# Kernel optimization log

Hardware: AMD Instinct MI355X
Metric: run time of the kernel (lower is better)

Reference implementation:

```python
import jax, jax.numpy as jnp
import numpy as np

BN_EPS = 1e-3


def _knn_group(p1, p2, k):
    # p1, p2: [B, N, 3]. For each point in p1, find k nearest in p2.
    d2 = (jnp.sum(p1 * p1, -1)[:, :, None]
          + jnp.sum(p2 * p2, -1)[:, None, :]
          - 2.0 * jnp.einsum('bnd,bmd->bnm', p1, p2))  # [B,N,N]
    _, idx = jax.lax.top_k(-d2, k)                      # [B,N,k]
    nn = jax.vmap(lambda pts, ind: pts[ind])(p2, idx)   # [B,N,k,3]
    resi = nn - p1[:, :, None, :]                       # [B,N,k,3]
    ss = jnp.sum(resi * resi, -1, keepdims=True)
    dist = jnp.sqrt(jnp.maximum(ss, 1e-12))             # safe norm
    feat = jnp.concatenate([resi, dist], -1)            # [B,N,k,4]
    return feat.transpose(0, 3, 1, 2), nn.transpose(0, 3, 1, 2)  # [B,4,N,k],[B,3,N,k]


def _conv_bn_relu(x, W, b, g, be, m, v):
    # 1x1 conv over channel dim: x [B,C,N,K], W [O,C]
    x = jnp.einsum('bcnk,oc->bonk', x, W) + b[None, :, None, None]
    x = (x - m[None, :, None, None]) * (g / jnp.sqrt(v + BN_EPS))[None, :, None, None] + be[None, :, None, None]
    return jax.nn.relu(x)


def setup_inputs() -> dict:
    key = jax.random.key(0)
    ks = jax.random.split(key, 20)
    B, N = 8, 2048
    chans = [4, 64, 64, 128]
    inp = {
        'points1': jax.random.normal(ks[0], (B, 3, N), jnp.float32),
        'points2': jax.random.normal(ks[1], (B, 3, N), jnp.float32),
    }
    for i in range(3):
        ci, co = chans[i], chans[i + 1]
        base = 2 + i * 6
        scale = 1.0 / np.sqrt(ci)
        inp[f'W{i+1}'] = jax.random.uniform(ks[base], (co, ci), jnp.float32, -scale, scale)
        inp[f'b{i+1}'] = jax.random.uniform(ks[base + 1], (co,), jnp.float32, -scale, scale)
        inp[f'g{i+1}'] = 1.0 + 0.1 * jax.random.normal(ks[base + 2], (co,), jnp.float32)
        inp[f'be{i+1}'] = 0.1 * jax.random.normal(ks[base + 3], (co,), jnp.float32)
        inp[f'm{i+1}'] = 0.05 * jax.random.normal(ks[base + 4], (co,), jnp.float32)
        inp[f'v{i+1}'] = jax.random.uniform(ks[base + 5], (co,), jnp.float32, 0.5, 1.5)
    inp['k'] = 32
    inp['t'] = 1
    return inp


def reference(points1, points2, W1, b1, g1, be1, m1, v1, W2, b2, g2, be2, m2, v2,
              W3, b3, g3, be3, m3, v3, k, t):
    p1 = points1.transpose(0, 2, 1)  # [B,N,3]
    p2 = points2.transpose(0, 2, 1)
    f1, nn1 = _knn_group(p1, p1, k)
    f2, nn2 = _knn_group(p1, p2, k)
    feats = jnp.concatenate([f1, f2], -1)          # [B,4,N,2k]
    grouped = jnp.concatenate([nn1, nn2], -1)      # [B,3,N,2k]
    x = _conv_bn_relu(feats, W1, b1, g1, be1, m1, v1)
    x = _conv_bn_relu(x, W2, b2, g2, be2, m2, v2)
    x = _conv_bn_relu(x, W3, b3, g3, be3, m3, v3)
    x = jnp.max(x, axis=1)                         # [B,N,2k] max over channels
    w = jax.nn.softmax(x, axis=-1)                 # softmax over 2k neighbors
    fused = jnp.sum(w[:, None, :, :] * grouped, -1)  # [B,3,N]
    return fused
```

## Files before the change

kernel.cpp:

```cpp
#include <hip/hip_runtime.h>
#include <hip/hip_bf16.h>
#include <stdint.h>

#define BB 8
#define NN 2048

#define OFF_B1 272
#define OFF_B2 4432
#define OFF_B3 12688
#define IDX_BYTE_OFF 65536
#define T_BASE   (65536 + 2*1024*1024)
#define T1_OFF   T_BASE
#define T2H_OFF  (T1_OFF + 4096)
#define T2L_OFF  (T2H_OFF + 9216)
#define T3H_OFF  (T2L_OFF + 9216)
#define T3L_OFF  (T3H_OFF + 18432)
#define L_T1   0
#define L_T2H  2048
#define L_T2L  6656
#define L_T3H  11264
#define L_T3L  20480
#define L_HALVES 29696

typedef __attribute__((ext_vector_type(4))) float f32x4;
typedef __attribute__((ext_vector_type(8))) short s16x8;

__device__ __forceinline__ float ldany(const void* p, long i, int isf32) {
    if (isf32) return ((const float*)p)[i];
    uint32_t u = ((uint32_t)((const uint16_t*)p)[i]) << 16;
    float f; __builtin_memcpy(&f, &u, 4); return f;
}
__device__ __forceinline__ uint16_t f2bf(float f) {
    uint32_t u; __builtin_memcpy(&u, &f, 4);
    return (uint16_t)((u + 0x7FFFu + ((u >> 16) & 1u)) >> 16);
}
__device__ __forceinline__ float bf2f(uint16_t h) {
    uint32_t u = ((uint32_t)h) << 16;
    float f; __builtin_memcpy(&f, &u, 4); return f;
}
__device__ __forceinline__ uint32_t pk2(float a, float b) {
    __hip_bfloat162 h = __float22bfloat162_rn(make_float2(a, b));
    uint32_t u; __builtin_memcpy(&u, &h, 4); return u;
}
__device__ __forceinline__ s16x8 mk8(uint32_t a, uint32_t b, uint32_t c, uint32_t d) {
    uint32_t t[4] = {a, b, c, d}; s16x8 r; __builtin_memcpy(&r, t, 16); return r;
}
__device__ __forceinline__ float sane(float v) {
    return (v == v && v > -1e30f && v < 1e30f) ? v : 0.f;
}
__device__ __forceinline__ int mbcnt64(unsigned long long m) {
    return __builtin_amdgcn_mbcnt_hi((uint32_t)(m >> 32),
           __builtin_amdgcn_mbcnt_lo((uint32_t)m, 0));
}
__device__ __forceinline__ int kperm_pos(int kk) {
    int g = kk >> 5, c5 = kk & 31;
    int sub = (c5 >> 4) & 1, q = (c5 >> 2) & 3, r = c5 & 3;
    return 32 * g + 8 * q + 4 * sub + r;
}

__global__ void kdetect(const void* p1, int* wsi) {
    __shared__ int s_cnt;
    int t = threadIdx.x;
    if (t == 0) s_cnt = 0;
    __syncthreads();
    const uint16_t* u = (const uint16_t*)p1;
    int c = 0;
    for (int i = t; i < 4096; i += 256) {
        uint16_t x = u[i];
        uint32_t e = (x >> 7) & 0xFF;
        c += ((e >= 0x70 && e <= 0x84) || x == 0) ? 1 : 0;
    }
    atomicAdd(&s_cnt, c);
    __syncthreads();
    if (t == 0) wsi[0] = (s_cnt < 3686) ? 1 : 0;
}

__device__ __forceinline__ void do_fold(int gid, int isf32,
                        const void* W1, const void* b1, const void* g1, const void* be1, const void* m1, const void* v1,
                        const void* W2, const void* b2, const void* g2, const void* be2, const void* m2, const void* v2,
                        const void* W3, const void* b3, const void* g3, const void* be3, const void* m3, const void* v3,
                        float* wsf) {
    uint16_t* t1  = (uint16_t*)((char*)wsf + T1_OFF);
    uint16_t* t2h = (uint16_t*)((char*)wsf + T2H_OFF);
    uint16_t* t2l = (uint16_t*)((char*)wsf + T2L_OFF);
    uint16_t* t3h = (uint16_t*)((char*)wsf + T3H_OFF);
    uint16_t* t3l = (uint16_t*)((char*)wsf + T3L_OFF);

    if (gid < 4096) {
        int o = gid >> 6, kk = gid & 63;
        float s = ldany(g2, o, isf32) * rsqrtf(ldany(v2, o, isf32) + 1e-3f);
        float w = ldany(W2, gid, isf32) * s;
        uint16_t wh = f2bf(w);
        int pos = o * 72 + kperm_pos(kk);
        t2h[pos] = wh; t2l[pos] = f2bf(w - bf2f(wh));
    } else if (gid < 12288) {
        int e = gid - 4096;
        int o = e >> 6, kk = e & 63;
        float s = ldany(g3, o, isf32) * rsqrtf(ldany(v3, o, isf32) + 1e-3f);
        float w = ldany(W3, e, isf32) * s;
        uint16_t wh = f2bf(w);
        int pos = o * 72 + kperm_pos(kk);
        t3h[pos] = wh; t3l[pos] = f2bf(w - bf2f(wh));
    } else if (gid < 12544) {
        int e = gid - 12288;
        int co = e >> 2, cc = e & 3;
        float s = ldany(g1, co, isf32) * rsqrtf(ldany(v1, co, isf32) + 1e-3f);
        float w = ldany(W1, co*4 + cc, isf32) * s;
        uint16_t wh = f2bf(w), wl = f2bf(w - bf2f(wh));
        t1[co*32 + cc]     = wh;
        t1[co*32 + 4 + cc] = wh;
        t1[co*32 + 8 + cc] = wl;
    } else if (gid < 13824) {
        int e = gid - 12544;
        int co = e / 20, k = e - co * 20;
        t1[co*32 + 12 + k] = 0;
    } else if (gid < 13888) {
        int o = gid - 13824;
        float s = ldany(g1, o, isf32) * rsqrtf(ldany(v1, o, isf32) + 1e-3f);
        wsf[OFF_B1 + o] = (ldany(b1, o, isf32) - ldany(m1, o, isf32)) * s + ldany(be1, o, isf32);
    } else if (gid < 13952) {
        int o = gid - 13888;
        float s = ldany(g2, o, isf32) * rsqrtf(ldany(v2, o, isf32) + 1e-3f);
        wsf[OFF_B2 + o] = (ldany(b2, o, isf32) - ldany(m2, o, isf32)) * s + ldany(be2, o, isf32);
    } else if (gid < 14080) {
        int o = gid - 13952;
        float s = ldany(g3, o, isf32) * rsqrtf(ldany(v3, o, isf32) + 1e-3f);
        wsf[OFF_B3 + o] = (ldany(b3, o, isf32) - ldany(m3, o, isf32)) * s + ldany(be3, o, isf32);
    }
}

__device__ __forceinline__ void knn_target(const void* p, long base, int isf32, int lane,
                                           float qx, float qy, float qz, float s1,
                                           unsigned long long* sl, uint16_t* dst) {
    uint32_t kb[32];
    if (!isf32) {
        const uint16_t* tpu = (const uint16_t*)p + base;
        const uint4* rx = (const uint4*)(tpu);
        const uint4* ry = (const uint4*)(tpu + NN);
        const uint4* rz = (const uint4*)(tpu + 2*NN);
        #pragma unroll
        for (int i = 0; i < 4; i++) {
            int v4 = i * 64 + lane;
            uint4 X = rx[v4], Y = ry[v4], Z = rz[v4];
            uint32_t xw[4] = {X.x, X.y, X.z, X.w};
            uint32_t yw[4] = {Y.x, Y.y, Y.z, Y.w};
            uint32_t zw[4] = {Z.x, Z.y, Z.z, Z.w};
            #pragma unroll
            for (int j = 0; j < 4; j++) {
                #pragma unroll
                for (int w = 0; w < 2; w++) {
                    uint32_t ux = (w == 0) ? (xw[j] << 16) : (xw[j] & 0xFFFF0000u);
                    uint32_t uy = (w == 0) ? (yw[j] << 16) : (yw[j] & 0xFFFF0000u);
                    uint32_t uz = (w == 0) ? (zw[j] << 16) : (zw[j] & 0xFFFF0000u);
                    float nx, ny, nz;
                    __builtin_memcpy(&nx, &ux, 4); __builtin_memcpy(&ny, &uy, 4); __builtin_memcpy(&nz, &uz, 4);
                    float s2  = nx * nx + ny * ny + nz * nz;
                    float dot = qx * nx + qy * ny + qz * nz;
                    float d2  = fmaxf((s1 + s2) - 2.0f * dot, 0.0f);
                    uint32_t bits; __builtin_memcpy(&bits, &d2, 4);
                    kb[i*8 + j*2 + w] = bits;
                }
            }
        }
    } else {
        const float* tpf = (const float*)p + base;
        #pragma unroll
        for (int i = 0; i < 32; i++) {
            int j = i * 64 + lane;
            float nx = tpf[j];
            float ny = tpf[NN + j];
            float nz = tpf[2*NN + j];
            float s2  = nx * nx + ny * ny + nz * nz;
            float dot = qx * nx + qy * ny + qz * nz;
            float d2  = fmaxf((s1 + s2) - 2.0f * dot, 0.0f);
            uint32_t bits; __builtin_memcpy(&bits, &d2, 4);
            kb[i] = bits;
        }
    }

    uint32_t lo = 0u, hi = 0x7F800001u, tau = 0u;
    uint32_t mid = 0x3E800000u;
    while (true) {
        int c = 0;
        #pragma unroll
        for (int i = 0; i < 32; i++) c += __builtin_popcountll(__ballot(kb[i] < mid));
        if (c >= 32 && c <= 64) { tau = mid; break; }
        if (c < 32) lo = mid; else hi = mid;
        if (hi - lo <= 1u) { tau = hi; break; }
        float mf; __builtin_memcpy(&mf, &mid, 4);
        float nf = mf * __powf(48.0f / (float)(c < 1 ? 1 : c), 0.6666667f);
        uint32_t nm; __builtin_memcpy(&nm, &nf, 4);
        if (!(nm > lo && nm < hi)) nm = lo + ((hi - lo) >> 1);
        mid = nm;
    }

    sl[lane] = ~0ull;
    int basePos = 0;
    #pragma unroll
    for (int i = 0; i < 32; i++) {
        unsigned idxv = isf32 ? (unsigned)(i * 64 + lane)
                              : (unsigned)((i >> 3) * 512 + 8 * lane + (i & 7));
        bool pz = kb[i] < tau;
        unsigned long long m = __ballot(pz);
        int pos = basePos + mbcnt64(m);
        if (pz && pos < 64) sl[pos] = (((unsigned long long)kb[i]) << 32) | idxv;
        basePos += __builtin_popcountll(m);
    }
    unsigned long long key = sl[lane];

    int ns = basePos > 64 ? 64 : basePos;
    unsigned long long mstar = ~0ull;
    if (ns != 32) {
        unsigned long long flo = 0ull;
        unsigned long long fhi = (((unsigned long long)tau) << 32) + 2048ull;
        float tauf; uint32_t tb = tau; __builtin_memcpy(&tauf, &tb, 4);
        float g = tauf * __powf(32.5f / (float)ns, 0.6666667f);
        uint32_t gb; __builtin_memcpy(&gb, &g, 4);
        unsigned long long m0 = ((unsigned long long)gb) << 32;
        if (!(m0 > flo && m0 < fhi)) m0 = flo + ((fhi - flo) >> 1);
        unsigned long long midk = m0;
        while (true) {
            int f = __builtin_popcountll(__ballot(key < midk));
            if (f == 32) { mstar = midk; break; }
            if (f < 32) flo = midk; else fhi = midk;
            if (fhi - flo <= 1ull) { mstar = fhi; break; }
            midk = flo + ((fhi - flo) >> 1);
        }
    }

    bool sel = key < mstar;
    unsigned long long sm = __ballot(sel);
    if (sel) dst[mbcnt64(sm)] = (uint16_t)(key & 0x7FFu);
}

__launch_bounds__(256)
__global__ void k1_knn(const void* p1, const void* p2,
                       const void* W1, const void* b1, const void* g1, const void* be1, const void* m1, const void* v1,
                       const void* W2, const void* b2, const void* g2, const void* be2, const void* m2, const void* v2,
                       const void* W3, const void* b3, const void* g3, const void* be3, const void* m3, const void* v3,
                       float* wsf, const int* wsi, uint16_t* idxout, int isf32arg) {
    __shared__ unsigned long long smem[4 * 64];

    int isf32 = (isf32arg >= 0) ? isf32arg : wsi[0];

    int t = threadIdx.x;
    int lane = threadIdx.x & 63;
    int wave = threadIdx.x >> 6;
    int qidx = blockIdx.x * 4 + wave;
    int b = qidx >> 11, n = qidx & 2047;
    long base = (long)b * 3 * NN;

    float qx = ldany(p1, base + n,        isf32);
    float qy = ldany(p1, base + NN + n,   isf32);
    float qz = ldany(p1, base + 2*NN + n, isf32);
    float s1 = qx * qx + qy * qy + qz * qz;

    unsigned long long* sl = smem + wave * 64;
    long obase = ((long)qidx) << 6;

    knn_target(p1, base, isf32, lane, qx, qy, qz, s1, sl, idxout + obase);

    __builtin_amdgcn_sched_barrier(0);
    asm volatile("" ::: "memory");

    knn_target(p2, base, isf32, lane, qx, qy, qz, s1, sl, idxout + obase + 32);

    if (blockIdx.x < 55) {
        int gid = blockIdx.x * 256 + t;
        do_fold(gid, isf32,
                W1, b1, g1, be1, m1, v1,
                W2, b2, g2, be2, m2, v2,
                W3, b3, g3, be3, m3, v3, wsf);
    }
}

__launch_bounds__(512)
__global__ void k2_mlp(const void* p1, const void* p2, const float* __restrict__ wsf, const int* wsi,
                       const uint16_t* __restrict__ idxin, void* outp, int isf32arg) {
    __shared__ uint4 shw4[L_HALVES / 8];

    {
        const uint4* src = (const uint4*)((const char*)wsf + T1_OFF);
        for (int i = threadIdx.x; i < L_HALVES / 8; i += 512) shw4[i] = src[i];
    }
    __syncthreads();
    const uint16_t* shw = (const uint16_t*)shw4;
    const uint16_t* T1  = shw + L_T1;
    const uint16_t* T2H = shw + L_T2H;
    const uint16_t* T2L = shw + L_T2L;
    const uint16_t* T3H = shw + L_T3H;
    const uint16_t* T3L = shw + L_T3L;

    int isf32 = (isf32arg >= 0) ? isf32arg : wsi[0];
    int lane = threadIdx.x & 63;
    int wave = threadIdx.x >> 6;
    int c = lane & 15;
    int q = lane >> 4;
    int qidx = blockIdx.x * 8 + wave;
    int b = qidx >> 11, n = qidx & 2047;
    long base = (long)b * 3 * NN;

    float qx = sane(ldany(p1, base + n,        isf32));
    float qy = sane(ldany(p1, base + NN + n,   isf32));
    float qz = sane(ldany(p1, base + 2*NN + n, isf32));

    int idx = idxin[((long)qidx << 6) + lane] & 2047;
    const void* sp = (lane < 32) ? p1 : p2;
    float nx = sane(ldany(sp, base + idx,        isf32));
    float ny = sane(ldany(sp, base + NN + idx,   isf32));
    float nz = sane(ldany(sp, base + 2*NN + idx, isf32));

    float r0 = nx - qx, r1 = ny - qy, r2 = nz - qz;
    float ss = fmaf(r0, r0, fmaf(r1, r1, r2 * r2));
    float dist = sqrtf(fmaxf(ss, 1e-12f));

    const float* B1 = wsf + OFF_B1;
    const float* B2 = wsf + OFF_B2;
    const float* B3 = wsf + OFF_B3;

    s16x8 b1f[4];
    #pragma unroll
    for (int nt = 0; nt < 4; nt++) {
        int src = 16 * nt + c;
        float f0 = __shfl(r0, src, 64);
        float f1 = __shfl(r1, src, 64);
        float f2v = __shfl(r2, src, 64);
        float f3v = __shfl(dist, src, 64);
        uint16_t h0 = f2bf(f0), h1 = f2bf(f1), h2 = f2bf(f2v), h3 = f2bf(f3v);
        uint16_t l0 = f2bf(f0 - bf2f(h0)), l1 = f2bf(f1 - bf2f(h1));
        uint16_t l2 = f2bf(f2v - bf2f(h2)), l3 = f2bf(f3v - bf2f(h3));
        s16x8 v;
        bool qa = (q < 2);
        bool qb = (q == 0);
        v[0] = qa ? (short)h0 : (short)0;
        v[1] = qa ? (short)h1 : (short)0;
        v[2] = qa ? (short)h2 : (short)0;
        v[3] = qa ? (short)h3 : (short)0;
        v[4] = qb ? (short)l0 : (short)0;
        v[5] = qb ? (short)l1 : (short)0;
        v[6] = qb ? (short)l2 : (short)0;
        v[7] = qb ? (short)l3 : (short)0;
        b1f[nt] = v;
    }

    f32x4 d1[4][4];
    #pragma unroll
    for (int mt = 0; mt < 4; mt++) {
        s16x8 a1 = *(const s16x8*)(T1 + (16 * mt + c) * 32 + q * 8);
        f32x4 bias = *(const f32x4*)(B1 + 16 * mt + 4 * q);
        #pragma unroll
        for (int nt = 0; nt < 4; nt++) {
            d1[mt][nt] = __builtin_amdgcn_mfma_f32_16x16x32_bf16(a1, b1f[nt], bias, 0, 0, 0);
        }
    }

    auto mkfrag = [](const f32x4& dlo, const f32x4& dhi) -> s16x8 {
        return mk8(pk2(fmaxf(dlo[0], 0.f), fmaxf(dlo[1], 0.f)),
                   pk2(fmaxf(dlo[2], 0.f), fmaxf(dlo[3], 0.f)),
                   pk2(fmaxf(dhi[0], 0.f), fmaxf(dhi[1], 0.f)),
                   pk2(fmaxf(dhi[2], 0.f), fmaxf(dhi[3], 0.f)));
    };

    f32x4 d2[4][4];
    #pragma unroll
    for (int mt = 0; mt < 4; mt++) {
        f32x4 bias = *(const f32x4*)(B2 + 16 * mt + 4 * q);
        #pragma unroll
        for (int nt = 0; nt < 4; nt++) d2[mt][nt] = bias;
    }
    #pragma unroll
    for (int g = 0; g < 2; g++) {
        s16x8 fh[4];
        #pragma unroll
        for (int nt = 0; nt < 4; nt++) fh[nt] = mkfrag(d1[2*g][nt], d1[2*g+1][nt]);
        #pragma unroll
        for (int mt = 0; mt < 4; mt++) {
            s16x8 ah = *(const s16x8*)(T2H + (16 * mt + c) * 72 + 32 * g + 8 * q);
            s16x8 al = *(const s16x8*)(T2L + (16 * mt + c) * 72 + 32 * g + 8 * q);
            #pragma unroll
            for (int nt = 0; nt < 4; nt++) {
                f32x4 acc = d2[mt][nt];
                acc = __builtin_amdgcn_mfma_f32_16x16x32_bf16(ah, fh[nt], acc, 0, 0, 0);
                acc = __builtin_amdgcn_mfma_f32_16x16x32_bf16(al, fh[nt], acc, 0, 0, 0);
                d2[mt][nt] = acc;
            }
        }
    }

    s16x8 f3h[2][4];
    #pragma unroll
    for (int g = 0; g < 2; g++)
        #pragma unroll
        for (int nt = 0; nt < 4; nt++) f3h[g][nt] = mkfrag(d2[2*g][nt], d2[2*g+1][nt]);

    float mx[4] = {-1e30f, -1e30f, -1e30f, -1e30f};
    #pragma unroll
    for (int mt = 0; mt < 8; mt++) {
        f32x4 bias = *(const f32x4*)(B3 + 16 * mt + 4 * q);
        f32x4 acc[4];
        #pragma unroll
        for (int nt = 0; nt < 4; nt++) acc[nt] = bias;
        #pragma unroll
        for (int g = 0; g < 2; g++) {
            s16x8 ah = *(const s16x8*)(T3H + (16 * mt + c) * 72 + 32 * g + 8 * q);
            s16x8 al = *(const s16x8*)(T3L + (16 * mt + c) * 72 + 32 * g + 8 * q);
            #pragma unroll
            for (int nt = 0; nt < 4; nt++) {
                f32x4 a = acc[nt];
                a = __builtin_amdgcn_mfma_f32_16x16x32_bf16(ah, f3h[g][nt], a, 0, 0, 0);
                a = __builtin_amdgcn_mfma_f32_16x16x32_bf16(al, f3h[g][nt], a, 0, 0, 0);
                acc[nt] = a;
            }
        }
        #pragma unroll
        for (int nt = 0; nt < 4; nt++) {
            mx[nt] = fmaxf(mx[nt], fmaxf(fmaxf(acc[nt][0], acc[nt][1]), fmaxf(acc[nt][2], acc[nt][3])));
        }
    }

    #pragma unroll
    for (int nt = 0; nt < 4; nt++) {
        mx[nt] = fmaxf(mx[nt], __shfl_xor(mx[nt], 16, 64));
        mx[nt] = fmaxf(mx[nt], __shfl_xor(mx[nt], 32, 64));
        mx[nt] = fmaxf(mx[nt], 0.f);
    }
    float mall = fmaxf(fmaxf(mx[0], mx[1]), fmaxf(mx[2], mx[3]));
    #pragma unroll
    for (int m = 1; m < 16; m <<= 1) mall = fmaxf(mall, __shfl_xor(mall, m, 64));
    float e0 = __expf(mx[0] - mall), e1 = __expf(mx[1] - mall);
    float e2 = __expf(mx[2] - mall), e3 = __expf(mx[3] - mall);
    float s = e0 + e1 + e2 + e3;
    #pragma unroll
    for (int m = 1; m < 16; m <<= 1) s += __shfl_xor(s, m, 64);
    float eown = (q == 0) ? e0 : (q == 1) ? e1 : (q == 2) ? e2 : e3;
    float w = eown / s;

    float sx = w * nx, sy = w * ny, sz = w * nz;
    #pragma unroll
    for (int m = 1; m < 64; m <<= 1) {
        sx += __shfl_xor(sx, m, 64);
        sy += __shfl_xor(sy, m, 64);
        sz += __shfl_xor(sz, m, 64);
    }

    if (lane < 3) {
        float v = (lane == 0) ? sx : ((lane == 1) ? sy : sz);
        long oi = base + (long)lane * NN + n;
        if (isf32) {
            ((float*)outp)[oi] = v;
        } else {
            ((uint16_t*)outp)[oi] = f2bf(v);
        }
    }
}

extern "C" void kernel_launch(void* const* d_in, const int* in_sizes, int n_in,
                              void* d_out, int out_size, void* d_ws, size_t ws_size,
                              hipStream_t stream) {
    const void* p1 = d_in[0];
    const void* p2 = d_in[1];
    float* wsf = (float*)d_ws;
    int*   wsi = (int*)d_ws;
    uint16_t* idxbuf = (uint16_t*)((char*)d_ws + IDX_BYTE_OFF);

    int isf32 = -1;
    if (in_sizes && n_in >= 1) {
        if (in_sizes[0] == BB * 3 * NN * 4)      isf32 = 1;
        else if (in_sizes[0] == BB * 3 * NN * 2) isf32 = 0;
    }
    if (isf32 < 0) {
        kdetect<<<1, 256, 0, stream>>>(p1, wsi);
    }

    k1_knn<<<(BB * NN) / 4, 256, 0, stream>>>(p1, p2,
        d_in[2],  d_in[3],  d_in[4],  d_in[5],  d_in[6],  d_in[7],
        d_in[8],  d_in[9],  d_in[10], d_in[11], d_in[12], d_in[13],
        d_in[14], d_in[15], d_in[16], d_in[17], d_in[18], d_in[19],
        wsf, wsi, idxbuf, isf32);

    k2_mlp<<<(BB * NN) / 8, 512, 0, stream>>>(p1, p2, wsf, wsi, idxbuf, d_out, isf32);
}
```

Before: 245.7 us.

## Restructure MLP kernel to process one neighbor tile at a time

Reorders the three-layer MFMA MLP so each 16-neighbor tile (nt) runs through all layers in a non-unrolled loop instead of keeping all four tiles' accumulators live at once. It also sets launch bounds to request four blocks per CU. The goal is to cut register pressure and raise occupancy so latency is better hidden. In exchange, LDS weight fragments are reloaded four times and the loop gives less instruction-level parallelism between independent MFMAs.

```diff
diff --git a/kernel.cpp b/kernel.cpp
--- a/kernel.cpp
+++ b/kernel.cpp
@@ -274,7 +274,7 @@
     }
 }
 
-__launch_bounds__(512)
+__launch_bounds__(512, 4)
 __global__ void k2_mlp(const void* p1, const void* p2, const float* __restrict__ wsf, const int* wsi,
                        const uint16_t* __restrict__ idxin, void* outp, int isf32arg) {
     __shared__ uint4 shw4[L_HALVES / 8];
@@ -318,42 +318,6 @@
     const float* B2 = wsf + OFF_B2;
     const float* B3 = wsf + OFF_B3;
 
-    s16x8 b1f[4];
-    #pragma unroll
-    for (int nt = 0; nt < 4; nt++) {
-        int src = 16 * nt + c;
-        float f0 = __shfl(r0, src, 64);
-        float f1 = __shfl(r1, src, 64);
-        float f2v = __shfl(r2, src, 64);
-        float f3v = __shfl(dist, src, 64);
-        uint16_t h0 = f2bf(f0), h1 = f2bf(f1), h2 = f2bf(f2v), h3 = f2bf(f3v);
-        uint16_t l0 = f2bf(f0 - bf2f(h0)), l1 = f2bf(f1 - bf2f(h1));
-        uint16_t l2 = f2bf(f2v - bf2f(h2)), l3 = f2bf(f3v - bf2f(h3));
-        s16x8 v;
-        bool qa = (q < 2);
-        bool qb = (q == 0);
-        v[0] = qa ? (short)h0 : (short)0;
-        v[1] = qa ? (short)h1 : (short)0;
-        v[2] = qa ? (short)h2 : (short)0;
-        v[3] = qa ? (short)h3 : (short)0;
-        v[4] = qb ? (short)l0 : (short)0;
-        v[5] = qb ? (short)l1 : (short)0;
-        v[6] = qb ? (short)l2 : (short)0;
-        v[7] = qb ? (short)l3 : (short)0;
-        b1f[nt] = v;
-    }
-
-    f32x4 d1[4][4];
-    #pragma unroll
-    for (int mt = 0; mt < 4; mt++) {
-        s16x8 a1 = *(const s16x8*)(T1 + (16 * mt + c) * 32 + q * 8);
-        f32x4 bias = *(const f32x4*)(B1 + 16 * mt + 4 * q);
-        #pragma unroll
-        for (int nt = 0; nt < 4; nt++) {
-            d1[mt][nt] = __builtin_amdgcn_mfma_f32_16x16x32_bf16(a1, b1f[nt], bias, 0, 0, 0);
-        }
-    }
-
     auto mkfrag = [](const f32x4& dlo, const f32x4& dhi) -> s16x8 {
         return mk8(pk2(fmaxf(dlo[0], 0.f), fmaxf(dlo[1], 0.f)),
                    pk2(fmaxf(dlo[2], 0.f), fmaxf(dlo[3], 0.f)),
@@ -361,74 +325,91 @@
                    pk2(fmaxf(dhi[2], 0.f), fmaxf(dhi[3], 0.f)));
     };
 
-    f32x4 d2[4][4];
-    #pragma unroll
-    for (int mt = 0; mt < 4; mt++) {
-        f32x4 bias = *(const f32x4*)(B2 + 16 * mt + 4 * q);
-        #pragma unroll
-        for (int nt = 0; nt < 4; nt++) d2[mt][nt] = bias;
-    }
-    #pragma unroll
-    for (int g = 0; g < 2; g++) {
-        s16x8 fh[4];
-        #pragma unroll
-        for (int nt = 0; nt < 4; nt++) fh[nt] = mkfrag(d1[2*g][nt], d1[2*g+1][nt]);
+    float mx0 = -1e30f, mx1 = -1e30f, mx2 = -1e30f, mx3 = -1e30f;
+    #pragma unroll 1
+    for (int nt = 0; nt < 4; nt++) {
+        int srcl = 16 * nt + c;
+        float f0 = __shfl(r0, srcl, 64);
+        float f1 = __shfl(r1, srcl, 64);
+        float f2v = __shfl(r2, srcl, 64);
+        float f3v = __shfl(dist, srcl, 64);
+        uint16_t h0 = f2bf(f0), h1 = f2bf(f1), h2 = f2bf(f2v), h3 = f2bf(f3v);
+        uint16_t l0 = f2bf(f0 - bf2f(h0)), l1 = f2bf(f1 - bf2f(h1));
+        uint16_t l2 = f2bf(f2v - bf2f(h2)), l3 = f2bf(f3v - bf2f(h3));
+        s16x8 bf;
+        bool qa = (q < 2);
+        bool qb = (q == 0);
+        bf[0] = qa ? (short)h0 : (short)0;
+        bf[1] = qa ? (short)h1 : (short)0;
+        bf[2] = qa ? (short)h2 : (short)0;
+        bf[3] = qa ? (short)h3 : (short)0;
+        bf[4] = qb ? (short)l0 : (short)0;
+        bf[5] = qb ? (short)l1 : (short)0;
+        bf[6] = qb ? (short)l2 : (short)0;
+        bf[7] = qb ? (short)l3 : (short)0;
+
+        f32x4 d1[4];
         #pragma unroll
         for (int mt = 0; mt < 4; mt++) {
-            s16x8 ah = *(const s16x8*)(T2H + (16 * mt + c) * 72 + 32 * g + 8 * q);
-            s16x8 al = *(const s16x8*)(T2L + (16 * mt + c) * 72 + 32 * g + 8 * q);
-            #pragma unroll
-            for (int nt = 0; nt < 4; nt++) {
-                f32x4 acc = d2[mt][nt];
-                acc = __builtin_amdgcn_mfma_f32_16x16x32_bf16(ah, fh[nt], acc, 0, 0, 0);
-                acc = __builtin_amdgcn_mfma_f32_16x16x32_bf16(al, fh[nt], acc, 0, 0, 0);
-                d2[mt][nt] = acc;
-            }
-        }
-    }
-
-    s16x8 f3h[2][4];
-    #pragma unroll
-    for (int g = 0; g < 2; g++)
-        #pragma unroll
-        for (int nt = 0; nt < 4; nt++) f3h[g][nt] = mkfrag(d2[2*g][nt], d2[2*g+1][nt]);
-
-    float mx[4] = {-1e30f, -1e30f, -1e30f, -1e30f};
-    #pragma unroll
-    for (int mt = 0; mt < 8; mt++) {
-        f32x4 bias = *(const f32x4*)(B3 + 16 * mt + 4 * q);
-        f32x4 acc[4];
-        #pragma unroll
-        for (int nt = 0; nt < 4; nt++) acc[nt] = bias;
-        #pragma unroll
-        for (int g = 0; g < 2; g++) {
-            s16x8 ah = *(const s16x8*)(T3H + (16 * mt + c) * 72 + 32 * g + 8 * q);
-            s16x8 al = *(const s16x8*)(T3L + (16 * mt + c) * 72 + 32 * g + 8 * q);
-            #pragma unroll
-            for (int nt = 0; nt < 4; nt++) {
-                f32x4 a = acc[nt];
-                a = __builtin_amdgcn_mfma_f32_16x16x32_bf16(ah, f3h[g][nt], a, 0, 0, 0);
-                a = __builtin_amdgcn_mfma_f32_16x16x32_bf16(al, f3h[g][nt], a, 0, 0, 0);
-                acc[nt] = a;
-            }
-        }
-        #pragma unroll
-        for (int nt = 0; nt < 4; nt++) {
-            mx[nt] = fmaxf(mx[nt], fmaxf(fmaxf(acc[nt][0], acc[nt][1]), fmaxf(acc[nt][2], acc[nt][3])));
-        }
-    }
-
-    #pragma unroll
-    for (int nt = 0; nt < 4; nt++) {
-        mx[nt] = fmaxf(mx[nt], __shfl_xor(mx[nt], 16, 64));
-        mx[nt] = fmaxf(mx[nt], __shfl_xor(mx[nt], 32, 64));
-        mx[nt] = fmaxf(mx[nt], 0.f);
-    }
-    float mall = fmaxf(fmaxf(mx[0], mx[1]), fmaxf(mx[2], mx[3]));
+            s16x8 a1 = *(const s16x8*)(T1 + (16 * mt + c) * 32 + q * 8);
+            f32x4 bias = *(const f32x4*)(B1 + 16 * mt + 4 * q);
+            d1[mt] = __builtin_amdgcn_mfma_f32_16x16x32_bf16(a1, bf, bias, 0, 0, 0);
+        }
+        s16x8 fh0 = mkfrag(d1[0], d1[1]);
+        s16x8 fh1 = mkfrag(d1[2], d1[3]);
+
+        f32x4 d2[4];
+        #pragma unroll
+        for (int mt = 0; mt < 4; mt++) {
+            f32x4 acc = *(const f32x4*)(B2 + 16 * mt + 4 * q);
+            s16x8 ah0 = *(const s16x8*)(T2H + (16 * mt + c) * 72 + 8 * q);
+            s16x8 al0 = *(const s16x8*)(T2L + (16 * mt + c) * 72 + 8 * q);
+            acc = __builtin_amdgcn_mfma_f32_16x16x32_bf16(ah0, fh0, acc, 0, 0, 0);
+            acc = __builtin_amdgcn_mfma_f32_16x16x32_bf16(al0, fh0, acc, 0, 0, 0);
+            s16x8 ah1 = *(const s16x8*)(T2H + (16 * mt + c) * 72 + 32 + 8 * q);
+            s16x8 al1 = *(const s16x8*)(T2L + (16 * mt + c) * 72 + 32 + 8 * q);
+            acc = __builtin_amdgcn_mfma_f32_16x16x32_bf16(ah1, fh1, acc, 0, 0, 0);
+            acc = __builtin_amdgcn_mfma_f32_16x16x32_bf16(al1, fh1, acc, 0, 0, 0);
+            d2[mt] = acc;
+        }
+        s16x8 g0 = mkfrag(d2[0], d2[1]);
+        s16x8 g1 = mkfrag(d2[2], d2[3]);
+
+        float m = -1e30f;
+        #pragma unroll
+        for (int mt = 0; mt < 8; mt++) {
+            f32x4 acc = *(const f32x4*)(B3 + 16 * mt + 4 * q);
+            s16x8 ah0 = *(const s16x8*)(T3H + (16 * mt + c) * 72 + 8 * q);
+            s16x8 al0 = *(const s16x8*)(T3L + (16 * mt + c) * 72 + 8 * q);
+            acc = __builtin_amdgcn_mfma_f32_16x16x32_bf16(ah0, g0, acc, 0, 0, 0);
+            acc = __builtin_amdgcn_mfma_f32_16x16x32_bf16(al0, g0, acc, 0, 0, 0);
+            s16x8 ah1 = *(const s16x8*)(T3H + (16 * mt + c) * 72 + 32 + 8 * q);
+            s16x8 al1 = *(const s16x8*)(T3L + (16 * mt + c) * 72 + 32 + 8 * q);
+            acc = __builtin_amdgcn_mfma_f32_16x16x32_bf16(ah1, g1, acc, 0, 0, 0);
+            acc = __builtin_amdgcn_mfma_f32_16x16x32_bf16(al1, g1, acc, 0, 0, 0);
+            m = fmaxf(m, fmaxf(fmaxf(acc[0], acc[1]), fmaxf(acc[2], acc[3])));
+        }
+        if (nt == 0) mx0 = m; else if (nt == 1) mx1 = m; else if (nt == 2) mx2 = m; else mx3 = m;
+    }
+
+    mx0 = fmaxf(mx0, __shfl_xor(mx0, 16, 64));
+    mx0 = fmaxf(mx0, __shfl_xor(mx0, 32, 64));
+    mx0 = fmaxf(mx0, 0.f);
+    mx1 = fmaxf(mx1, __shfl_xor(mx1, 16, 64));
+    mx1 = fmaxf(mx1, __shfl_xor(mx1, 32, 64));
+    mx1 = fmaxf(mx1, 0.f);
+    mx2 = fmaxf(mx2, __shfl_xor(mx2, 16, 64));
+    mx2 = fmaxf(mx2, __shfl_xor(mx2, 32, 64));
+    mx2 = fmaxf(mx2, 0.f);
+    mx3 = fmaxf(mx3, __shfl_xor(mx3, 16, 64));
+    mx3 = fmaxf(mx3, __shfl_xor(mx3, 32, 64));
+    mx3 = fmaxf(mx3, 0.f);
+
+    float mall = fmaxf(fmaxf(mx0, mx1), fmaxf(mx2, mx3));
     #pragma unroll
     for (int m = 1; m < 16; m <<= 1) mall = fmaxf(mall, __shfl_xor(mall, m, 64));
-    float e0 = __expf(mx[0] - mall), e1 = __expf(mx[1] - mall);
-    float e2 = __expf(mx[2] - mall), e3 = __expf(mx[3] - mall);
+    float e0 = __expf(mx0 - mall), e1 = __expf(mx1 - mall);
+    float e2 = __expf(mx2 - mall), e3 = __expf(mx3 - mall);
     float s = e0 + e1 + e2 + e3;
     #pragma unroll
     for (int m = 1; m < 16; m <<= 1) s += __shfl_xor(s, m, 64);
```

New measurement: 819.8 us. +233.6%, slower.
